# Kernel tuning notes

Hardware: AMD Instinct MI355X
Metric: run time of the kernel (lower is better)

Reference implementation:

```python
import jax, jax.numpy as jnp
import numpy as np

B, S, H = 2, 2048, 1024
NH, HD = 16, 64  # num_heads, head_dim


def setup_inputs() -> dict:
    key = jax.random.key(0)
    k1, k2, k3 = jax.random.split(key, 3)
    return {
        "hidden_states": jax.random.normal(k1, (B, S, H), dtype=jnp.float32),
        "attention_mask": jnp.zeros((B, S), dtype=jnp.float32),
        "w_qkv": jax.random.normal(k2, (3 * H, H), dtype=jnp.float32) * (1.0 / np.sqrt(H)),
        "b_qkv": jnp.zeros((3 * H,), dtype=jnp.float32),
        "w_out": jax.random.normal(k3, (H, H), dtype=jnp.float32) * (1.0 / np.sqrt(H)),
        "b_out": jnp.zeros((H,), dtype=jnp.float32),
    }


def reference(hidden_states, attention_mask, w_qkv, b_qkv, w_out, b_out):
    scale = HD ** -0.5
    qkv = hidden_states @ w_qkv.T + b_qkv          # [B,S,3H]
    qkv = qkv.reshape(B, S, 3, NH, HD)
    qkv = jnp.transpose(qkv, (2, 0, 3, 1, 4))      # [3,B,NH,S,HD]
    q, k, v = qkv[0], qkv[1], qkv[2]
    scores = jnp.einsum("bhqd,bhkd->bhqk", q, k) * scale
    # 2D additive mask broadcast to [B,1,1,S] as in torch unsqueeze path
    scores = scores + attention_mask[:, None, None, :]
    attn = jax.nn.softmax(scores, axis=-1)
    out = jnp.einsum("bhqk,bhkd->bhqd", attn, v)   # [B,NH,S,HD]
    out = jnp.transpose(out, (0, 2, 1, 3)).reshape(B, S, H)
    return out @ w_out.T + b_out
```

## Files before the change

kernel.cpp:

```cpp
#include <hip/hip_runtime.h>
#include <stdint.h>

typedef short bfrag __attribute__((ext_vector_type(8)));
typedef float f32x4 __attribute__((ext_vector_type(4)));

#define LOG2E 1.4426950408889634f

__device__ __forceinline__ ushort f2bf(float x){
  union { float f; uint32_t u; } c; c.f = x;
  uint32_t r = (c.u + 0x7fffu + ((c.u >> 16) & 1u)) >> 16;
  return (ushort)r;
}

__device__ __forceinline__ uint32_t cvt_pk_bf16(float lo, float hi){
  uint32_t r;
  asm("v_cvt_pk_bf16_f32 %0, %1, %2" : "=v"(r) : "v"(lo), "v"(hi));
  return r;
}

__device__ __forceinline__ void load_lds16(const void* g, void* l){
  __builtin_amdgcn_global_load_lds((const __attribute__((address_space(1))) void*)g,
                                   (__attribute__((address_space(3))) void*)l,
                                   16, 0, 0);
}

template<int CTRL>
__device__ __forceinline__ float dppf(float x){
  return __builtin_bit_cast(float, __builtin_amdgcn_update_dpp(
      0, __builtin_bit_cast(int, x), CTRL, 0xf, 0xf, true));
}
__device__ __forceinline__ float rowmax16(float x){
  x = fmaxf(x, dppf<0x128>(x));
  x = fmaxf(x, dppf<0x124>(x));
  x = fmaxf(x, dppf<0x122>(x));
  x = fmaxf(x, dppf<0x121>(x));
  return x;
}
__device__ __forceinline__ float rowsum16(float x){
  x += dppf<0x128>(x);
  x += dppf<0x124>(x);
  x += dppf<0x122>(x);
  x += dppf<0x121>(x);
  return x;
}

__global__ void cast_all(const float* __restrict__ hs, const float* __restrict__ wqkv,
                         const float* __restrict__ wout, ushort* __restrict__ out){
  const int i = blockIdx.x * blockDim.x + threadIdx.x;
  float4 f;
  if (i < 1048576)       f = ((const float4*)hs)[i];
  else if (i < 1835008)  f = ((const float4*)wqkv)[i - 1048576];
  else                   f = ((const float4*)wout)[i - 1835008];
  ushort4 u;
  u.x = f2bf(f.x); u.y = f2bf(f.y); u.z = f2bf(f.z); u.w = f2bf(f.w);
  ((ushort4*)out)[i] = u;
}

__global__ __launch_bounds__(256)
void transpose_v(const ushort* __restrict__ v, ushort* __restrict__ vt){
  __shared__ ushort T[64*64];
  const int t = threadIdx.x;
  const int bh = blockIdx.y, s0 = blockIdx.x * 64;
  const ushort* vb = v + ((size_t)bh * 2048 + s0) * 64;
  ushort* vtb = vt + (size_t)bh * 64 * 2048 + s0;
#pragma unroll
  for (int i = 0; i < 2; i++){
    const int s = (t >> 3) + i*32, c = (t & 7) * 8;
    bfrag x = *(const bfrag*)(vb + (size_t)s * 64 + c);
    *(bfrag*)((char*)T + ((s*128 + c*2) ^ (((s >> 3) & 7) << 4))) = x;
  }
  __syncthreads();
#pragma unroll
  for (int i = 0; i < 2; i++){
    const int d = (t >> 3) + i*32, c = (t & 7) * 8;
    bfrag y;
#pragma unroll
    for (int j = 0; j < 8; j++){
      const int s = c + j;
      y[j] = *(const ushort*)((char*)T + ((s*128 + d*2) ^ (((s >> 3) & 7) << 4)));
    }
    *(bfrag*)(vtb + (size_t)d * 2048 + c) = y;
  }
}

template<int EPI>
__global__ __launch_bounds__(256)
void gemm_bt(const ushort* __restrict__ A, const ushort* __restrict__ B,
             const float* __restrict__ bias,
             ushort* __restrict__ dq, ushort* __restrict__ dk, ushort* __restrict__ dv,
             float* __restrict__ dout,
             int M, int N, int K)
{
  __shared__ ushort Alds[2][128*32];
  __shared__ ushort Blds[2][128*32];
  const int t = threadIdx.x;
  const int w = t >> 6, l = t & 63;
  const int lr = l & 15, lg = l >> 4;
  const int m0 = blockIdx.x * 128, n0 = blockIdx.y * 128;
  const int wm = (w >> 1) * 64, wn = (w & 1) * 64;

  f32x4 acc[4][4] = {};

  auto stage = [&](int buf, int kt){
#pragma unroll
    for (int i = 0; i < 2; i++){
      const int row = i*64 + w*16 + (l >> 2);
      const int ce  = (l & 3) * 8;
      load_lds16(A + (size_t)(m0 + row) * K + kt*32 + ce, &Alds[buf][(i*64 + w*16) * 32]);
      load_lds16(B + (size_t)(n0 + row) * K + kt*32 + ce, &Blds[buf][(i*64 + w*16) * 32]);
    }
  };

  const int nk = K >> 5;
  int cur = 0;
  stage(0, 0);
  __syncthreads();
  for (int kt = 0; kt < nk; kt++){
    if (kt + 1 < nk) stage(cur ^ 1, kt + 1);
    bfrag af[4], bfv[4];
#pragma unroll
    for (int f = 0; f < 4; f++){
      af[f]  = *(const bfrag*)&Alds[cur][(wm + f*16 + lr) * 32 + lg * 8];
      bfv[f] = *(const bfrag*)&Blds[cur][(wn + f*16 + lr) * 32 + lg * 8];
    }
#pragma unroll
    for (int mf = 0; mf < 4; mf++)
#pragma unroll
      for (int nf = 0; nf < 4; nf++)
        acc[mf][nf] = __builtin_amdgcn_mfma_f32_16x16x32_bf16(af[mf], bfv[nf], acc[mf][nf], 0, 0, 0);
    __syncthreads();
    cur ^= 1;
  }

#pragma unroll
  for (int mf = 0; mf < 4; mf++){
#pragma unroll
    for (int nf = 0; nf < 4; nf++){
      const int col = n0 + wn + nf*16 + lr;
      const float bs = bias[col];
#pragma unroll
      for (int r = 0; r < 4; r++){
        const int row = m0 + wm + mf*16 + lg*4 + r;
        const float vv = acc[mf][nf][r] + bs;
        if (EPI == 1){
          const int which = col >> 10;
          const int hd = col & 1023;
          const int bb = row >> 11, s = row & 2047;
          const int bh = (bb << 4) + (hd >> 6);
          ushort* dst = (which == 0) ? dq : (which == 1) ? dk : dv;
          dst[((size_t)bh * 2048 + s) * 64 + (hd & 63)] = f2bf(vv);
        } else {
          dout[(size_t)row * N + col] = vv;
        }
      }
    }
  }
}

__global__ __launch_bounds__(512, 4)
void flash_attn(const ushort* __restrict__ q, const ushort* __restrict__ k,
                const ushort* __restrict__ vt, const float* __restrict__ mask,
                ushort* __restrict__ ao)
{
  __shared__ ushort Klds[2][64*64];
  __shared__ ushort Vlds[2][64*64];
  __shared__ ushort Plds[8][16*64];
  const int t = threadIdx.x;
  const int w = t >> 6, l = t & 63;
  const int lr = l & 15, lg = l >> 4;
  const int bh = blockIdx.y;
  const int b = bh >> 4, h = bh & 15;
  const int q0 = blockIdx.x * 128;
  const ushort* qb  = q  + (size_t)bh * 2048 * 64;
  const ushort* kb  = k  + (size_t)bh * 2048 * 64;
  const ushort* vtb = vt + (size_t)bh * 64 * 2048;
  const float* mb = mask + b * 2048;

  const int srow = t >> 3;
  const int spc  = (t & 7) * 16;

  auto stageKV = [&](int buf, int kv0){
    const int off = spc ^ ((srow & 7) << 4);
    load_lds16((const char*)(kb + (size_t)kv0 * 64) + srow*128 + off,
               (char*)&Klds[buf][0] + w*1024);
    load_lds16((const char*)vtb + (size_t)srow * 4096 + kv0*2 + off,
               (char*)&Vlds[buf][0] + w*1024);
  };

  bfrag qf[2];
#pragma unroll
  for (int kf = 0; kf < 2; kf++){
    const int row = q0 + w*16 + lr;
    qf[kf] = *(const bfrag*)(qb + (size_t)row * 64 + kf*32 + lg*8);
  }

  float mrun[4], lsum[4];
  f32x4 oacc[4] = {};
#pragma unroll
  for (int r = 0; r < 4; r++){ mrun[r] = -1e30f; lsum[r] = 0.f; }

  const float SC2 = 0.125f * LOG2E;

  stageKV(0, 0);
  float mk[4], mkn[4] = {0.f, 0.f, 0.f, 0.f};
#pragma unroll
  for (int nf = 0; nf < 4; nf++) mk[nf] = mb[nf*16 + lr] * LOG2E;

  int cur = 0;
  for (int kv0 = 0; kv0 < 2048; kv0 += 64){
    __syncthreads();
    if (kv0 + 64 < 2048){
      stageKV(cur ^ 1, kv0 + 64);
#pragma unroll
      for (int nf = 0; nf < 4; nf++) mkn[nf] = mb[kv0 + 64 + nf*16 + lr] * LOG2E;
    }

    bfrag bk[4][2];
#pragma unroll
    for (int nf = 0; nf < 4; nf++)
#pragma unroll
      for (int kf = 0; kf < 2; kf++){
        const int row = nf*16 + lr;
        const int kbyte = kf*64 + lg*16;
        bk[nf][kf] = *(const bfrag*)((const char*)&Klds[cur][0] + row*128 + (kbyte ^ ((row & 7) << 4)));
      }
    f32x4 sa[4] = {};
#pragma unroll
    for (int nf = 0; nf < 4; nf++)
#pragma unroll
      for (int kf = 0; kf < 2; kf++)
        sa[nf] = __builtin_amdgcn_mfma_f32_16x16x32_bf16(qf[kf], bk[nf][kf], sa[nf], 0, 0, 0);

    float sc[4][4], mx4[4];
#pragma unroll
    for (int r = 0; r < 4; r++){
#pragma unroll
      for (int nf = 0; nf < 4; nf++) sc[r][nf] = sa[nf][r]*SC2 + mk[nf];
      mx4[r] = fmaxf(fmaxf(sc[r][0], sc[r][1]), fmaxf(sc[r][2], sc[r][3]));
    }

    const bool grew = (mx4[0] > mrun[0] + 8.f) | (mx4[1] > mrun[1] + 8.f) |
                      (mx4[2] > mrun[2] + 8.f) | (mx4[3] > mrun[3] + 8.f);
    if (__any(grew)){
#pragma unroll
      for (int r = 0; r < 4; r++){
        const float mnew = fmaxf(mrun[r], rowmax16(mx4[r]));
        const float c = __builtin_amdgcn_exp2f(mrun[r] - mnew);
        mrun[r] = mnew;
        lsum[r] *= c;
#pragma unroll
        for (int nf = 0; nf < 4; nf++) oacc[nf][r] *= c;
      }
    }

#pragma unroll
    for (int r = 0; r < 4; r++){
      const float p0 = __builtin_amdgcn_exp2f(sc[r][0] - mrun[r]);
      const float p1 = __builtin_amdgcn_exp2f(sc[r][1] - mrun[r]);
      const float p2 = __builtin_amdgcn_exp2f(sc[r][2] - mrun[r]);
      const float p3 = __builtin_amdgcn_exp2f(sc[r][3] - mrun[r]);
      lsum[r] += (p0 + p1) + (p2 + p3);
      const uint32_t w01 = cvt_pk_bf16(p0, p1);
      const uint32_t w23 = cvt_pk_bf16(p2, p3);
      const int prow = lg*4 + r;
      const int sw = (prow & 7) << 4;
      char* pbase = (char*)&Plds[w][0] + prow*128;
      *(ushort*)(pbase + ((lr*2      ) ^ sw)) = (ushort)w01;
      *(ushort*)(pbase + ((lr*2 + 32 ) ^ sw)) = (ushort)(w01 >> 16);
      *(ushort*)(pbase + ((lr*2 + 64 ) ^ sw)) = (ushort)w23;
      *(ushort*)(pbase + ((lr*2 + 96 ) ^ sw)) = (ushort)(w23 >> 16);
    }

    bfrag bv[4][2], ap[2];
#pragma unroll
    for (int nf = 0; nf < 4; nf++)
#pragma unroll
      for (int kf = 0; kf < 2; kf++){
        const int d = nf*16 + lr;
        const int kbyte = kf*64 + lg*16;
        bv[nf][kf] = *(const bfrag*)((const char*)&Vlds[cur][0] + d*128 + (kbyte ^ ((d & 7) << 4)));
      }
#pragma unroll
    for (int kf = 0; kf < 2; kf++){
      const int kbyte = kf*64 + lg*16;
      ap[kf] = *(const bfrag*)((const char*)&Plds[w][0] + lr*128 + (kbyte ^ ((lr & 7) << 4)));
    }
#pragma unroll
    for (int nf = 0; nf < 4; nf++)
#pragma unroll
      for (int kf = 0; kf < 2; kf++)
        oacc[nf] = __builtin_amdgcn_mfma_f32_16x16x32_bf16(ap[kf], bv[nf][kf], oacc[nf], 0, 0, 0);

#pragma unroll
    for (int nf = 0; nf < 4; nf++) mk[nf] = mkn[nf];
    cur ^= 1;
  }

#pragma unroll
  for (int r = 0; r < 4; r++){
    const float inv = 1.f / rowsum16(lsum[r]);
#pragma unroll
    for (int nf = 0; nf < 4; nf++){
      const int grow = b*2048 + q0 + w*16 + lg*4 + r;
      const int col = h*64 + nf*16 + lr;
      ao[(size_t)grow * 1024 + col] = f2bf(oacc[nf][r] * inv);
    }
  }
}

extern "C" void kernel_launch(void* const* d_in, const int* in_sizes, int n_in,
                              void* d_out, int out_size, void* d_ws, size_t ws_size,
                              hipStream_t stream)
{
  (void)in_sizes; (void)n_in; (void)out_size; (void)ws_size;
  const float* hs   = (const float*)d_in[0];
  const float* mask = (const float*)d_in[1];
  const float* wqkv = (const float*)d_in[2];
  const float* bqkv = (const float*)d_in[3];
  const float* wout = (const float*)d_in[4];
  const float* bout = (const float*)d_in[5];
  float* out = (float*)d_out;

  char* ws = (char*)d_ws;
  ushort* hs_bf = (ushort*)(ws);
  ushort* w1_bf = (ushort*)(ws + 8388608);
  ushort* w2_bf = (ushort*)(ws + 14680064);
  ushort* q_bf  = (ushort*)(ws + 16777216);
  ushort* k_bf  = (ushort*)(ws + 25165824);
  ushort* v_bf  = (ushort*)(ws + 33554432);
  ushort* vt_bf = (ushort*)(ws + 41943040);
  ushort* ao_bf = (ushort*)(ws + 50331648);

  cast_all<<<8192, 256, 0, stream>>>(hs, wqkv, wout, (ushort*)ws);

  gemm_bt<1><<<dim3(32, 24), 256, 0, stream>>>(hs_bf, w1_bf, bqkv,
                                               q_bf, k_bf, v_bf, nullptr,
                                               4096, 3072, 1024);
  transpose_v<<<dim3(32, 32), 256, 0, stream>>>(v_bf, vt_bf);
  flash_attn<<<dim3(16, 32), 512, 0, stream>>>(q_bf, k_bf, vt_bf, mask, ao_bf);
  gemm_bt<2><<<dim3(32, 8), 256, 0, stream>>>(ao_bf, w2_bf, bout,
                                              nullptr, nullptr, nullptr, out,
                                              4096, 1024, 1024);
}
```

Measured before the change: 136.0 us.

## Compute transposed S in flash attention so P stays in registers, skip LDS round-trip

```diff
diff --git a/kernel.cpp b/kernel.cpp
--- a/kernel.cpp
+++ b/kernel.cpp
@@ -3,8 +3,11 @@
 
 typedef short bfrag __attribute__((ext_vector_type(8)));
 typedef float f32x4 __attribute__((ext_vector_type(4)));
+typedef uint  uint4v __attribute__((ext_vector_type(4)));
+typedef uint  uint2v __attribute__((ext_vector_type(2)));
 
 #define LOG2E 1.4426950408889634f
+#define SWZ(row) ((((row) & 3) | (((row) >> 1) & 4)) << 4)
 
 __device__ __forceinline__ ushort f2bf(float x){
   union { float f; uint32_t u; } c; c.f = x;
@@ -18,42 +21,41 @@
   return r;
 }
 
+__device__ __forceinline__ float redq_max(float x){
+  x = fmaxf(x, __shfl_xor(x, 16));
+  x = fmaxf(x, __shfl_xor(x, 32));
+  return x;
+}
+__device__ __forceinline__ float redq_sum(float x){
+  x += __shfl_xor(x, 16);
+  x += __shfl_xor(x, 32);
+  return x;
+}
+
 __device__ __forceinline__ void load_lds16(const void* g, void* l){
   __builtin_amdgcn_global_load_lds((const __attribute__((address_space(1))) void*)g,
                                    (__attribute__((address_space(3))) void*)l,
                                    16, 0, 0);
 }
 
-template<int CTRL>
-__device__ __forceinline__ float dppf(float x){
-  return __builtin_bit_cast(float, __builtin_amdgcn_update_dpp(
-      0, __builtin_bit_cast(int, x), CTRL, 0xf, 0xf, true));
-}
-__device__ __forceinline__ float rowmax16(float x){
-  x = fmaxf(x, dppf<0x128>(x));
-  x = fmaxf(x, dppf<0x124>(x));
-  x = fmaxf(x, dppf<0x122>(x));
-  x = fmaxf(x, dppf<0x121>(x));
-  return x;
-}
-__device__ __forceinline__ float rowsum16(float x){
-  x += dppf<0x128>(x);
-  x += dppf<0x124>(x);
-  x += dppf<0x122>(x);
-  x += dppf<0x121>(x);
-  return x;
-}
-
 __global__ void cast_all(const float* __restrict__ hs, const float* __restrict__ wqkv,
-                         const float* __restrict__ wout, ushort* __restrict__ out){
+                         const float* __restrict__ wout, const float* __restrict__ mask,
+                         ushort* __restrict__ out, float* __restrict__ mask2){
   const int i = blockIdx.x * blockDim.x + threadIdx.x;
-  float4 f;
-  if (i < 1048576)       f = ((const float4*)hs)[i];
-  else if (i < 1835008)  f = ((const float4*)wqkv)[i - 1048576];
-  else                   f = ((const float4*)wout)[i - 1835008];
-  ushort4 u;
-  u.x = f2bf(f.x); u.y = f2bf(f.y); u.z = f2bf(f.z); u.w = f2bf(f.w);
-  ((ushort4*)out)[i] = u;
+  if (i < 2097152){
+    float4 f;
+    if (i < 1048576)       f = ((const float4*)hs)[i];
+    else if (i < 1835008)  f = ((const float4*)wqkv)[i - 1048576];
+    else                   f = ((const float4*)wout)[i - 1835008];
+    ushort4 u;
+    u.x = f2bf(f.x); u.y = f2bf(f.y); u.z = f2bf(f.z); u.w = f2bf(f.w);
+    ((ushort4*)out)[i] = u;
+  } else {
+    const int j = i - 2097152;
+    float4 m = ((const float4*)mask)[j];
+    m.x *= LOG2E; m.y *= LOG2E; m.z *= LOG2E; m.w *= LOG2E;
+    ((float4*)mask2)[j] = m;
+  }
 }
 
 __global__ __launch_bounds__(256)
@@ -159,12 +161,11 @@
 
 __global__ __launch_bounds__(512, 4)
 void flash_attn(const ushort* __restrict__ q, const ushort* __restrict__ k,
-                const ushort* __restrict__ vt, const float* __restrict__ mask,
+                const ushort* __restrict__ vt, const float* __restrict__ mask2,
                 ushort* __restrict__ ao)
 {
   __shared__ ushort Klds[2][64*64];
   __shared__ ushort Vlds[2][64*64];
-  __shared__ ushort Plds[8][16*64];
   const int t = threadIdx.x;
   const int w = t >> 6, l = t & 63;
   const int lr = l & 15, lg = l >> 4;
@@ -174,16 +175,15 @@
   const ushort* qb  = q  + (size_t)bh * 2048 * 64;
   const ushort* kb  = k  + (size_t)bh * 2048 * 64;
   const ushort* vtb = vt + (size_t)bh * 64 * 2048;
-  const float* mb = mask + b * 2048;
+  const float* mb = mask2 + b * 2048;
 
   const int srow = t >> 3;
-  const int spc  = (t & 7) * 16;
+  const int soff = ((t & 7) * 16) ^ SWZ(srow);
 
   auto stageKV = [&](int buf, int kv0){
-    const int off = spc ^ ((srow & 7) << 4);
-    load_lds16((const char*)(kb + (size_t)kv0 * 64) + srow*128 + off,
+    load_lds16((const char*)(kb + (size_t)kv0 * 64) + srow*128 + soff,
                (char*)&Klds[buf][0] + w*1024);
-    load_lds16((const char*)vtb + (size_t)srow * 4096 + kv0*2 + off,
+    load_lds16((const char*)vtb + (size_t)srow * 4096 + kv0*2 + soff,
                (char*)&Vlds[buf][0] + w*1024);
   };
 
@@ -194,117 +194,112 @@
     qf[kf] = *(const bfrag*)(qb + (size_t)row * 64 + kf*32 + lg*8);
   }
 
-  float mrun[4], lsum[4];
+  float mrun = -1e30f, lsum = 0.f;
   f32x4 oacc[4] = {};
-#pragma unroll
-  for (int r = 0; r < 4; r++){ mrun[r] = -1e30f; lsum[r] = 0.f; }
 
   const float SC2 = 0.125f * LOG2E;
+  const int rbase = (lr >> 2) * 8 + (lr & 3);
 
   stageKV(0, 0);
-  float mk[4], mkn[4] = {0.f, 0.f, 0.f, 0.f};
-#pragma unroll
-  for (int nf = 0; nf < 4; nf++) mk[nf] = mb[nf*16 + lr] * LOG2E;
 
   int cur = 0;
   for (int kv0 = 0; kv0 < 2048; kv0 += 64){
     __syncthreads();
-    if (kv0 + 64 < 2048){
-      stageKV(cur ^ 1, kv0 + 64);
-#pragma unroll
-      for (int nf = 0; nf < 4; nf++) mkn[nf] = mb[kv0 + 64 + nf*16 + lr] * LOG2E;
-    }
+    if (kv0 + 64 < 2048) stageKV(cur ^ 1, kv0 + 64);
+
+    float4 mk[4];
+#pragma unroll
+    for (int nf = 0; nf < 4; nf++)
+      mk[nf] = *(const float4*)(mb + kv0 + ((nf & 1) << 5) + (lg << 3) + ((nf >> 1) << 2));
 
     bfrag bk[4][2];
 #pragma unroll
-    for (int nf = 0; nf < 4; nf++)
+    for (int nf = 0; nf < 4; nf++){
+      const int rho = ((nf & 1) << 5) + ((nf >> 1) << 2) + rbase;
+      const int rsw = SWZ(rho);
 #pragma unroll
       for (int kf = 0; kf < 2; kf++){
-        const int row = nf*16 + lr;
         const int kbyte = kf*64 + lg*16;
-        bk[nf][kf] = *(const bfrag*)((const char*)&Klds[cur][0] + row*128 + (kbyte ^ ((row & 7) << 4)));
+        bk[nf][kf] = *(const bfrag*)((const char*)&Klds[cur][0] + rho*128 + (kbyte ^ rsw));
       }
+    }
     f32x4 sa[4] = {};
 #pragma unroll
     for (int nf = 0; nf < 4; nf++)
 #pragma unroll
       for (int kf = 0; kf < 2; kf++)
-        sa[nf] = __builtin_amdgcn_mfma_f32_16x16x32_bf16(qf[kf], bk[nf][kf], sa[nf], 0, 0, 0);
-
-    float sc[4][4], mx4[4];
-#pragma unroll
-    for (int r = 0; r < 4; r++){
-#pragma unroll
-      for (int nf = 0; nf < 4; nf++) sc[r][nf] = sa[nf][r]*SC2 + mk[nf];
-      mx4[r] = fmaxf(fmaxf(sc[r][0], sc[r][1]), fmaxf(sc[r][2], sc[r][3]));
-    }
-
-    const bool grew = (mx4[0] > mrun[0] + 8.f) | (mx4[1] > mrun[1] + 8.f) |
-                      (mx4[2] > mrun[2] + 8.f) | (mx4[3] > mrun[3] + 8.f);
-    if (__any(grew)){
+        sa[nf] = __builtin_amdgcn_mfma_f32_16x16x32_bf16(bk[nf][kf], qf[kf], sa[nf], 0, 0, 0);
+
+    float sc[4][4];
+#pragma unroll
+    for (int nf = 0; nf < 4; nf++){
+      sc[nf][0] = fmaf(sa[nf][0], SC2, mk[nf].x);
+      sc[nf][1] = fmaf(sa[nf][1], SC2, mk[nf].y);
+      sc[nf][2] = fmaf(sa[nf][2], SC2, mk[nf].z);
+      sc[nf][3] = fmaf(sa[nf][3], SC2, mk[nf].w);
+    }
+    float mx = sc[0][0];
+#pragma unroll
+    for (int nf = 0; nf < 4; nf++)
+#pragma unroll
+      for (int r = 0; r < 4; r++) mx = fmaxf(mx, sc[nf][r]);
+
+    if (__any(mx > mrun + 8.f)){
+      const float mnew = fmaxf(mrun, redq_max(mx));
+      const float c = __builtin_amdgcn_exp2f(mrun - mnew);
+      mrun = mnew;
+      lsum *= c;
+#pragma unroll
+      for (int nf = 0; nf < 4; nf++) oacc[nf] *= c;
+    }
+
+    float p[4][4];
+    float ps = 0.f;
+#pragma unroll
+    for (int nf = 0; nf < 4; nf++)
 #pragma unroll
       for (int r = 0; r < 4; r++){
-        const float mnew = fmaxf(mrun[r], rowmax16(mx4[r]));
-        const float c = __builtin_amdgcn_exp2f(mrun[r] - mnew);
-        mrun[r] = mnew;
-        lsum[r] *= c;
-#pragma unroll
-        for (int nf = 0; nf < 4; nf++) oacc[nf][r] *= c;
+        p[nf][r] = __builtin_amdgcn_exp2f(sc[nf][r] - mrun);
+        ps += p[nf][r];
       }
-    }
-
-#pragma unroll
-    for (int r = 0; r < 4; r++){
-      const float p0 = __builtin_amdgcn_exp2f(sc[r][0] - mrun[r]);
-      const float p1 = __builtin_amdgcn_exp2f(sc[r][1] - mrun[r]);
-      const float p2 = __builtin_amdgcn_exp2f(sc[r][2] - mrun[r]);
-      const float p3 = __builtin_amdgcn_exp2f(sc[r][3] - mrun[r]);
-      lsum[r] += (p0 + p1) + (p2 + p3);
-      const uint32_t w01 = cvt_pk_bf16(p0, p1);
-      const uint32_t w23 = cvt_pk_bf16(p2, p3);
-      const int prow = lg*4 + r;
-      const int sw = (prow & 7) << 4;
-      char* pbase = (char*)&Plds[w][0] + prow*128;
-      *(ushort*)(pbase + ((lr*2      ) ^ sw)) = (ushort)w01;
-      *(ushort*)(pbase + ((lr*2 + 32 ) ^ sw)) = (ushort)(w01 >> 16);
-      *(ushort*)(pbase + ((lr*2 + 64 ) ^ sw)) = (ushort)w23;
-      *(ushort*)(pbase + ((lr*2 + 96 ) ^ sw)) = (ushort)(w23 >> 16);
-    }
-
-    bfrag bv[4][2], ap[2];
+    lsum += ps;
+
+    bfrag ap[2];
+#pragma unroll
+    for (int kf = 0; kf < 2; kf++){
+      uint4v tv = { cvt_pk_bf16(p[kf][0],   p[kf][1]),
+                    cvt_pk_bf16(p[kf][2],   p[kf][3]),
+                    cvt_pk_bf16(p[kf+2][0], p[kf+2][1]),
+                    cvt_pk_bf16(p[kf+2][2], p[kf+2][3]) };
+      ap[kf] = __builtin_bit_cast(bfrag, tv);
+    }
+
+    bfrag bv[4][2];
 #pragma unroll
     for (int nf = 0; nf < 4; nf++)
 #pragma unroll
       for (int kf = 0; kf < 2; kf++){
         const int d = nf*16 + lr;
         const int kbyte = kf*64 + lg*16;
-        bv[nf][kf] = *(const bfrag*)((const char*)&Vlds[cur][0] + d*128 + (kbyte ^ ((d & 7) << 4)));
+        bv[nf][kf] = *(const bfrag*)((const char*)&Vlds[cur][0] + d*128 + (kbyte ^ SWZ(d)));
       }
 #pragma unroll
-    for (int kf = 0; kf < 2; kf++){
-      const int kbyte = kf*64 + lg*16;
-      ap[kf] = *(const bfrag*)((const char*)&Plds[w][0] + lr*128 + (kbyte ^ ((lr & 7) << 4)));
-    }
-#pragma unroll
     for (int nf = 0; nf < 4; nf++)
 #pragma unroll
       for (int kf = 0; kf < 2; kf++)
-        oacc[nf] = __builtin_amdgcn_mfma_f32_16x16x32_bf16(ap[kf], bv[nf][kf], oacc[nf], 0, 0, 0);
-
-#pragma unroll
-    for (int nf = 0; nf < 4; nf++) mk[nf] = mkn[nf];
+        oacc[nf] = __builtin_amdgcn_mfma_f32_16x16x32_bf16(bv[nf][kf], ap[kf], oacc[nf], 0, 0, 0);
+
     cur ^= 1;
   }
 
-#pragma unroll
-  for (int r = 0; r < 4; r++){
-    const float inv = 1.f / rowsum16(lsum[r]);
-#pragma unroll
-    for (int nf = 0; nf < 4; nf++){
-      const int grow = b*2048 + q0 + w*16 + lg*4 + r;
-      const int col = h*64 + nf*16 + lr;
-      ao[(size_t)grow * 1024 + col] = f2bf(oacc[nf][r] * inv);
-    }
+  const float inv = 1.f / redq_sum(lsum);
+  ushort* orow = ao + (size_t)(b*2048 + q0 + w*16 + lr) * 1024 + h*64 + lg*4;
+#pragma unroll
+  for (int nf = 0; nf < 4; nf++){
+    const uint32_t w01 = cvt_pk_bf16(oacc[nf][0] * inv, oacc[nf][1] * inv);
+    const uint32_t w23 = cvt_pk_bf16(oacc[nf][2] * inv, oacc[nf][3] * inv);
+    uint2v vv = {w01, w23};
+    *(uint2v*)(orow + nf*16) = vv;
   }
 }
 
@@ -330,14 +325,15 @@
   ushort* v_bf  = (ushort*)(ws + 33554432);
   ushort* vt_bf = (ushort*)(ws + 41943040);
   ushort* ao_bf = (ushort*)(ws + 50331648);
-
-  cast_all<<<8192, 256, 0, stream>>>(hs, wqkv, wout, (ushort*)ws);
+  float*  mask2 = (float*)(ws + 58720256);
+
+  cast_all<<<8196, 256, 0, stream>>>(hs, wqkv, wout, mask, (ushort*)ws, mask2);
 
   gemm_bt<1><<<dim3(32, 24), 256, 0, stream>>>(hs_bf, w1_bf, bqkv,
                                                q_bf, k_bf, v_bf, nullptr,
                                                4096, 3072, 1024);
   transpose_v<<<dim3(32, 32), 256, 0, stream>>>(v_bf, vt_bf);
-  flash_attn<<<dim3(16, 32), 512, 0, stream>>>(q_bf, k_bf, vt_bf, mask, ao_bf);
+  flash_attn<<<dim3(16, 32), 512, 0, stream>>>(q_bf, k_bf, vt_bf, mask2, ao_bf);
   gemm_bt<2><<<dim3(32, 8), 256, 0, stream>>>(ao_bf, w2_bf, bout,
                                               nullptr, nullptr, nullptr, out,
                                               4096, 1024, 1024);
```

New measurement: 128.6 us. -5.5%, faster.
